# Optimization experiments

Hardware: AMD Instinct MI355X
Metric: run time of the kernel (lower is better)

Reference implementation:

```python
import jax, jax.numpy as jnp
import numpy as np
from jax import lax

B, N, C = 8, 100000, 90
H = W = 512
CONF_THR = 0.25
IOU_THR = 0.45
MAX_DET = 100  # fixed-size padded replacement for dynamic per-image NMS output


def setup_inputs() -> dict:
    key = jax.random.key(0)
    k1, k2, k3, k4, k5 = jax.random.split(key, 5)
    # small deltas so exp(dw), exp(dh) stay sane
    regression = jax.random.normal(k1, (B, N, 4), jnp.float32) * 0.1
    # shifted logits so sigmoid scores are mostly below conf_threshold (realistic sparsity)
    classification = jax.random.normal(k2, (B, N, C), jnp.float32) * 2.0 - 4.0
    # anchors in (y1, x1, y2, x2), valid boxes inside a 512x512 canvas
    cy = jax.random.uniform(k3, (1, N), minval=0.0, maxval=float(H))
    cx = jax.random.uniform(k4, (1, N), minval=0.0, maxval=float(W))
    hw = jax.random.uniform(k5, (1, N, 2), minval=16.0, maxval=128.0)
    hh, ww = hw[..., 0], hw[..., 1]
    anchors = jnp.stack([cy - hh / 2, cx - ww / 2, cy + hh / 2, cx + ww / 2], axis=-1)
    imgs = jnp.zeros((B, 3, H, W), jnp.float32)  # only shape (H, W) is used
    return {"regression": regression, "classification": classification,
            "anchors": anchors, "imgs": imgs}


def _bbox_transform(anchors, regression):
    y_c_a = (anchors[..., 0] + anchors[..., 2]) / 2
    x_c_a = (anchors[..., 1] + anchors[..., 3]) / 2
    ha = anchors[..., 2] - anchors[..., 0]
    wa = anchors[..., 3] - anchors[..., 1]
    w = jnp.exp(regression[..., 3]) * wa
    h = jnp.exp(regression[..., 2]) * ha
    y_c = regression[..., 0] * ha + y_c_a
    x_c = regression[..., 1] * wa + x_c_a
    # output in (x1, y1, x2, y2)
    return jnp.stack([x_c - w / 2, y_c - h / 2, x_c + w / 2, y_c + h / 2], axis=-1)


def _clip_boxes(boxes, height, width):
    x = jnp.clip(boxes[..., 0::2], 0.0, float(width))
    y = jnp.clip(boxes[..., 1::2], 0.0, float(height))
    return jnp.stack([x[..., 0], y[..., 0], x[..., 1], y[..., 1]], axis=-1)


def _iou_one_vs_all(box, boxes):
    # box [4], boxes [N,4] in x1y1x2y2
    x1 = jnp.maximum(box[0], boxes[:, 0])
    y1 = jnp.maximum(box[1], boxes[:, 1])
    x2 = jnp.minimum(box[2], boxes[:, 2])
    y2 = jnp.minimum(box[3], boxes[:, 3])
    inter = jnp.clip(x2 - x1, 0.0) * jnp.clip(y2 - y1, 0.0)
    area = (box[2] - box[0]) * (box[3] - box[1])
    areas = (boxes[:, 2] - boxes[:, 0]) * (boxes[:, 3] - boxes[:, 1])
    return inter / (area + areas - inter + 1e-8)


def _process_image(boxes, cls_logits):
    # boxes [N,4], cls_logits [N,C]
    scores_all = jax.nn.sigmoid(cls_logits)
    max_scores = jnp.max(scores_all, axis=1)
    labels = jnp.argmax(scores_all, axis=1)
    # below-threshold anchors get -1 so they can never be selected (== torch pre-NMS filter)
    s0 = jnp.where(max_scores > CONF_THR, max_scores, -1.0)
    s0 = lax.stop_gradient(s0)
    boxes_sg = lax.stop_gradient(boxes)

    def step(sc, _):
        best = jnp.argmax(sc)
        valid = sc[best] > 0.0
        iou = _iou_one_vs_all(boxes_sg[best], boxes_sg)
        sc = jnp.where(valid & (iou > IOU_THR), -1.0, sc)
        sc = sc.at[best].set(-1.0)
        return sc, jnp.where(valid, best, -1)

    _, idx = lax.scan(step, s0, None, length=MAX_DET)  # [MAX_DET] int
    valid = idx >= 0
    idx_safe = jnp.maximum(idx, 0)
    out_scores = jnp.where(valid, max_scores[idx_safe], 0.0)
    out_labels = jnp.where(valid, labels[idx_safe], -1)
    out_boxes = jnp.where(valid[:, None], boxes[idx_safe], 0.0)
    return out_scores, out_labels, out_boxes


def reference(regression, classification, anchors, imgs):
    height, width = imgs.shape[2], imgs.shape[3]
    boxes = _bbox_transform(anchors, regression)          # [B,N,4]
    boxes = _clip_boxes(boxes, height, width)
    scores, labels, det_boxes = jax.vmap(_process_image)(boxes, classification)
    # padded outputs: scores [B,MAX_DET], labels [B,MAX_DET] (-1 = invalid), boxes [B,MAX_DET,4]
    return scores, labels, det_boxes
```

## Files before the change

### kernel.cpp

```cpp
#include <hip/hip_runtime.h>

#define NB 8
#define NA 100000
#define NC 90
#define MAXDET 100
#define KCAND 2048
#define NBINS 4096
#define NBLK 13
#define BLK_ANCH 8000
#define ABLK 128
#define MASK_WORDS 32
#define CH_ROWS 64
#define CONF 0.25f
#define IOUT 0.45f

static constexpr size_t OFF_SCORE = 0;
static constexpr size_t OFF_LABEL = OFF_SCORE + (size_t)NB * NA * 4;
static constexpr size_t OFF_HROWS = OFF_LABEL + (size_t)NB * NA;
static constexpr size_t OFF_THR   = OFF_HROWS + (size_t)NB * NBLK * NBINS * 4;
static constexpr size_t OFF_CNT   = OFF_THR + 64;
static constexpr size_t OFF_CKEY  = OFF_CNT + 64;
static constexpr size_t OFF_SSC   = OFF_CKEY + (size_t)NB * KCAND * 8;
static constexpr size_t OFF_SLAB  = OFF_SSC + (size_t)NB * KCAND * 4;
static constexpr size_t OFF_SBOX  = OFF_SLAB + (size_t)NB * KCAND * 4;
static constexpr size_t OFF_MASK  = OFF_SBOX + (size_t)NB * KCAND * 16;

__device__ __forceinline__ float4 decode_clip(float4 a, float4 r) {
#pragma clang fp contract(off)
    float yca = (a.x + a.z) * 0.5f;
    float xca = (a.y + a.w) * 0.5f;
    float ha  = a.z - a.x;
    float wa  = a.w - a.y;
    float w   = expf(r.w) * wa;
    float h   = expf(r.z) * ha;
    float yc  = r.x * ha + yca;
    float xc  = r.y * wa + xca;
    float x1  = xc - w * 0.5f, y1 = yc - h * 0.5f;
    float x2  = xc + w * 0.5f, y2 = yc + h * 0.5f;
    x1 = fminf(fmaxf(x1, 0.0f), 512.0f);
    x2 = fminf(fmaxf(x2, 0.0f), 512.0f);
    y1 = fminf(fmaxf(y1, 0.0f), 512.0f);
    y2 = fminf(fmaxf(y2, 0.0f), 512.0f);
    return make_float4(x1, y1, x2, y2);
}

__global__ __launch_bounds__(256) void k_score_box(const float* __restrict__ cls,
                                                   float* __restrict__ ws_score,
                                                   unsigned char* __restrict__ ws_label) {
    __shared__ float tile[ABLK * NC];
    int t = threadIdx.x;
    const float4* g4 = (const float4*)(cls + (size_t)blockIdx.x * (ABLK * NC));
    float4* t4 = (float4*)tile;
    for (int i = t; i < ABLK * NC / 4; i += 256) t4[i] = g4[i];
    __syncthreads();

    int la = t >> 1, h = t & 1;
    const float* row = tile + la * NC + h * 45;
    int jbase = NC - 1 - h * 45;
    unsigned long long best = 0ULL;
    for (int j2 = 0; j2 < 45; ++j2) {
        float x = row[j2];
        float s = 1.0f / (1.0f + expf(-x));
        unsigned long long key = ((unsigned long long)__float_as_uint(s) << 32) |
                                 (unsigned long long)(unsigned)(jbase - j2);
        if (key > best) best = key;
    }
    unsigned long long o = __shfl_xor(best, 1, 64);
    if (o > best) best = o;
    if (h == 0) {
        int a = blockIdx.x * ABLK + la;
        ws_score[a] = __uint_as_float((unsigned)(best >> 32));
        ws_label[a] = (unsigned char)(NC - 1 - (unsigned)(best & 0xFFFFFFFFu));
    }
}

__global__ __launch_bounds__(256) void k_hist(const float* __restrict__ ws_score,
                                              unsigned* __restrict__ hrows) {
    __shared__ unsigned h[NBINS];
    int b = blockIdx.y, blk = blockIdx.x, tid = threadIdx.x;
    for (int i = tid; i < NBINS; i += 256) h[i] = 0u;
    __syncthreads();
    int base = blk * BLK_ANCH;
    int lim = min(BLK_ANCH, NA - base);
    const float* sc = ws_score + (size_t)b * NA + base;
    for (int i = tid; i < lim; i += 256) {
        float s = sc[i];
        if (s > CONF) {
            int bin = min((int)(s * (float)NBINS), NBINS - 1);
            atomicAdd(&h[bin], 1u);
        }
    }
    __syncthreads();
    unsigned* row = hrows + ((size_t)b * NBLK + blk) * NBINS;
    for (int i = tid; i < NBINS; i += 256) row[i] = h[i];
}

__global__ __launch_bounds__(256) void k_thresh(const unsigned* __restrict__ hrows,
                                                unsigned* __restrict__ thr_bin,
                                                unsigned* __restrict__ cnt) {
    __shared__ unsigned h[NBINS];
    __shared__ unsigned chunk[256];
    __shared__ int bstar;
    int b = blockIdx.x, t = threadIdx.x;
    for (int i = t; i < NBINS; i += 256) {
        unsigned s = 0;
        for (int r = 0; r < NBLK; ++r) s += hrows[((size_t)b * NBLK + r) * NBINS + i];
        h[i] = s;
    }
    if (t == 0) { bstar = NBINS - 1; cnt[b] = 0u; }
    __syncthreads();
    unsigned s = 0;
    for (int j = 0; j < 16; ++j) s += h[t * 16 + j];
    chunk[t] = s;
    __syncthreads();
    unsigned U = 0;
    for (int j = t + 1; j < 256; ++j) U += chunk[j];
    unsigned run = U;
    int cand = NBINS;
    for (int j = 15; j >= 0; --j) {
        run += h[t * 16 + j];
        if (run <= (unsigned)KCAND) cand = t * 16 + j;
    }
    if (cand < NBINS) atomicMin(&bstar, cand);
    __syncthreads();
    if (t == 0) thr_bin[b] = (unsigned)bstar;
}

__global__ __launch_bounds__(256) void k_compact(const float* __restrict__ ws_score,
                                                 const unsigned* __restrict__ thr_bin,
                                                 unsigned* __restrict__ cnt,
                                                 unsigned long long* __restrict__ ckey) {
    __shared__ unsigned scan[256];
    __shared__ unsigned base_s;
    int b = blockIdx.y, blk = blockIdx.x, t = threadIdx.x;
    int base = blk * BLK_ANCH;
    int lim = min(BLK_ANCH, NA - base);
    size_t ibase = (size_t)b * NA + base;
    unsigned thr = thr_bin[b];

    unsigned c = 0;
    for (int i = t; i < lim; i += 256) {
        float s = ws_score[ibase + i];
        if (s > CONF) {
            int bin = min((int)(s * (float)NBINS), NBINS - 1);
            if ((unsigned)bin >= thr) c++;
        }
    }
    scan[t] = c;
    __syncthreads();
    for (int off = 1; off < 256; off <<= 1) {
        unsigned v = (t >= off) ? scan[t - off] : 0u;
        __syncthreads();
        scan[t] += v;
        __syncthreads();
    }
    if (t == 255) base_s = atomicAdd(&cnt[b], scan[255]);
    __syncthreads();
    unsigned pos = base_s + scan[t] - c;
    for (int i = t; i < lim; i += 256) {
        float s = ws_score[ibase + i];
        if (s > CONF) {
            int bin = min((int)(s * (float)NBINS), NBINS - 1);
            if ((unsigned)bin >= thr) {
                unsigned p = pos++;
                if (p < (unsigned)KCAND) {
                    int n = base + i;
                    ckey[(size_t)b * KCAND + p] =
                        ((unsigned long long)__float_as_uint(s) << 32) |
                        (unsigned long long)(0xFFFFFFFFu - (unsigned)n);
                }
            }
        }
    }
}

__global__ __launch_bounds__(256) void k_sortdecode(const unsigned long long* __restrict__ ckey,
                                                    const unsigned* __restrict__ cnt,
                                                    const unsigned char* __restrict__ ws_label,
                                                    const float* __restrict__ reg,
                                                    const float* __restrict__ anc,
                                                    float* __restrict__ sscore,
                                                    int* __restrict__ slab,
                                                    float4* __restrict__ sbox) {
    __shared__ unsigned long long key[KCAND];
    int b = blockIdx.x, t = threadIdx.x;
    unsigned M = min(cnt[b], (unsigned)KCAND);
    for (int i = t; i < KCAND; i += 256)
        key[i] = (i < (int)M) ? ckey[(size_t)b * KCAND + i] : 0ULL;
    __syncthreads();
    for (int k = 2; k <= KCAND; k <<= 1) {
        for (int j = k >> 1; j > 0; j >>= 1) {
            for (int s = 0; s < KCAND / 256; ++s) {
                int p = t + s * 256;
                int q = p ^ j;
                if (q > p) {
                    unsigned long long a = key[p], bb = key[q];
                    bool desc = ((p & k) == 0);
                    if (desc ? (a < bb) : (a > bb)) { key[p] = bb; key[q] = a; }
                }
            }
            __syncthreads();
        }
    }
    for (int i = t; i < KCAND; i += 256) {
        unsigned long long kk = key[i];
        size_t o = (size_t)b * KCAND + i;
        if (kk != 0ULL) {
            unsigned n = 0xFFFFFFFFu - (unsigned)(kk & 0xFFFFFFFFu);
            sscore[o] = __uint_as_float((unsigned)(kk >> 32));
            slab[o] = (int)ws_label[(size_t)b * NA + n];
            float4 a4 = ((const float4*)anc)[n];
            float4 r4 = ((const float4*)reg)[(size_t)b * NA + n];
            sbox[o] = decode_clip(a4, r4);
        } else {
            sscore[o] = 0.0f;
            slab[o] = -1;
            sbox[o] = make_float4(0.f, 0.f, 0.f, 0.f);
        }
    }
}

__global__ __launch_bounds__(256) void k_mask(const float4* __restrict__ sbox,
                                              unsigned long long* __restrict__ mask) {
    __shared__ float4 bx[KCAND];
    int b = blockIdx.y, t = threadIdx.x;
    for (int i = t; i < KCAND; i += 256) bx[i] = sbox[(size_t)b * KCAND + i];
    __syncthreads();
    int r = t >> 5, w = t & 31;
    int row = blockIdx.x * 8 + r;
    float4 rb = bx[row];
    unsigned long long bits = 0ULL;
    {
#pragma clang fp contract(off)
        float areaR = (rb.z - rb.x) * (rb.w - rb.y);
        int cbase = w * 64;
        for (int cc = 0; cc < 64; ++cc) {
            float4 cb = bx[cbase + cc];
            float x1 = fmaxf(rb.x, cb.x), y1 = fmaxf(rb.y, cb.y);
            float x2 = fminf(rb.z, cb.z), y2 = fminf(rb.w, cb.w);
            float inter = fmaxf(x2 - x1, 0.0f) * fmaxf(y2 - y1, 0.0f);
            float areaC = (cb.z - cb.x) * (cb.w - cb.y);
            float iou = inter / (areaR + areaC - inter + 1e-8f);
            if (iou > IOUT) bits |= (1ULL << cc);
        }
    }
    mask[((size_t)b * KCAND + row) * MASK_WORDS + w] = bits;
}

__global__ __launch_bounds__(256) void k_scan(const unsigned long long* __restrict__ mask,
                                              const unsigned* __restrict__ cnt,
                                              const float* __restrict__ sscore,
                                              const int* __restrict__ slab,
                                              const float4* __restrict__ sbox,
                                              float* __restrict__ out) {
    __shared__ unsigned long long buf[2][CH_ROWS * MASK_WORDS];
    __shared__ int picks[MAXDET];
    __shared__ int npick_s;
    __shared__ int done_s;

    int b = blockIdx.x, t = threadIdx.x;
    unsigned M = min(cnt[b], (unsigned)KCAND);
    const unsigned long long* mbase = mask + (size_t)b * KCAND * MASK_WORDS;

    if (t == 0) { npick_s = 0; done_s = 0; }
    for (int i = t; i < CH_ROWS * MASK_WORDS; i += 256) buf[0][i] = mbase[i];
    __syncthreads();

    unsigned long long removed = 0ULL;
    int npick = 0;

    for (int q = 0; q < KCAND / CH_ROWS; ++q) {
        int cur = q & 1;
        bool havepre = (q + 1 < KCAND / CH_ROWS) && !done_s;
        unsigned long long pre[CH_ROWS * MASK_WORDS / 256];
        if (havepre) {
            const unsigned long long* src = mbase + (size_t)(q + 1) * CH_ROWS * MASK_WORDS;
#pragma unroll
            for (int s = 0; s < CH_ROWS * MASK_WORDS / 256; ++s) pre[s] = src[t + s * 256];
        }
        if (t < 64) {
            const unsigned long long* ch = buf[cur];
            int gstart = q * 64;
            if (gstart < (int)M && npick < MAXDET) {
                int vg = (int)M - gstart;
                unsigned long long valid = (vg >= 64) ? ~0ULL : ((1ULL << vg) - 1ULL);
                while (npick < MAXDET) {
                    unsigned long long rg = __shfl(removed, q, 64);
                    unsigned long long free = ~rg & valid;
                    if (free == 0ULL) break;
                    int cl = __ffsll((long long)free) - 1;
                    int c = gstart + cl;
                    if (t == 0) picks[npick] = c;
                    npick++;
                    if (t == q) removed |= (1ULL << cl);
                    if (t < 32) removed |= ch[cl * MASK_WORDS + t];
                }
            }
            if (t == 0) {
                npick_s = npick;
                done_s = (npick >= MAXDET || (q + 1) * CH_ROWS >= (int)M) ? 1 : 0;
            }
        }
        if (havepre) {
#pragma unroll
            for (int s = 0; s < CH_ROWS * MASK_WORDS / 256; ++s)
                buf[1 - cur][t + s * 256] = pre[s];
        }
        __syncthreads();
        if (done_s) break;
    }

    __syncthreads();
    int np = npick_s;
    for (int k = t; k < MAXDET; k += 256) {
        float sc = 0.0f, lb = -1.0f;
        float4 bb = make_float4(0.f, 0.f, 0.f, 0.f);
        if (k < np) {
            int i = picks[k];
            size_t o = (size_t)b * KCAND + i;
            sc = sscore[o];
            lb = (float)slab[o];
            bb = sbox[o];
        }
        out[b * MAXDET + k] = sc;
        out[NB * MAXDET + b * MAXDET + k] = lb;
        ((float4*)(out + 2 * NB * MAXDET))[b * MAXDET + k] = bb;
    }
}

extern "C" void kernel_launch(void* const* d_in, const int* in_sizes, int n_in,
                              void* d_out, int out_size, void* d_ws, size_t ws_size,
                              hipStream_t stream) {
    const float* reg = (const float*)d_in[0];
    const float* cls = (const float*)d_in[1];
    const float* anc = (const float*)d_in[2];

    char* ws = (char*)d_ws;
    float* ws_score           = (float*)(ws + OFF_SCORE);
    unsigned char* ws_label   = (unsigned char*)(ws + OFF_LABEL);
    unsigned* hrows           = (unsigned*)(ws + OFF_HROWS);
    unsigned* thr_bin         = (unsigned*)(ws + OFF_THR);
    unsigned* cnt             = (unsigned*)(ws + OFF_CNT);
    unsigned long long* ckey  = (unsigned long long*)(ws + OFF_CKEY);
    float* sscore             = (float*)(ws + OFF_SSC);
    int* slab                 = (int*)(ws + OFF_SLAB);
    float4* sbox              = (float4*)(ws + OFF_SBOX);
    unsigned long long* maskp = (unsigned long long*)(ws + OFF_MASK);

    float* out = (float*)d_out;

    k_score_box<<<NB * NA / ABLK, 256, 0, stream>>>(cls, ws_score, ws_label);
    k_hist<<<dim3(NBLK, NB), 256, 0, stream>>>(ws_score, hrows);
    k_thresh<<<NB, 256, 0, stream>>>(hrows, thr_bin, cnt);
    k_compact<<<dim3(NBLK, NB), 256, 0, stream>>>(ws_score, thr_bin, cnt, ckey);
    k_sortdecode<<<NB, 256, 0, stream>>>(ckey, cnt, ws_label, reg, anc, sscore, slab, sbox);
    k_mask<<<dim3(KCAND / 8, NB), 256, 0, stream>>>(sbox, maskp);
    k_scan<<<NB, 256, 0, stream>>>(maskp, cnt, sscore, slab, sbox, out);
}
```

Baseline: 608.0 us.

## Split score rows across four threads, widen sort block, simplify NMS scan

The score kernel now uses 64 anchors per block with four threads per anchor row and a two-step shuffle max, giving more blocks and shorter per-thread loops. The bitonic sort runs with 1024 threads per image instead of 256, so each thread does fewer compare-exchanges per stage. The NMS scan is replaced by a single-wave kernel that picks the next survivor with a ballot and reads mask rows straight from global memory, dropping the double-buffered shared-memory chunking. This removes barriers in the scan, but each pick now waits on a dependent global load.

New measurement: 580.7 us. 4.5% less time.

```diff
diff --git a/kernel.cpp b/kernel.cpp
--- a/kernel.cpp
+++ b/kernel.cpp
@@ -8,9 +8,8 @@
 #define NBINS 4096
 #define NBLK 13
 #define BLK_ANCH 8000
-#define ABLK 128
+#define ABLK 64
 #define MASK_WORDS 32
-#define CH_ROWS 64
 #define CONF 0.25f
 #define IOUT 0.45f
 
@@ -51,21 +50,25 @@
     int t = threadIdx.x;
     const float4* g4 = (const float4*)(cls + (size_t)blockIdx.x * (ABLK * NC));
     float4* t4 = (float4*)tile;
+#pragma unroll
     for (int i = t; i < ABLK * NC / 4; i += 256) t4[i] = g4[i];
     __syncthreads();
 
-    int la = t >> 1, h = t & 1;
-    const float* row = tile + la * NC + h * 45;
-    int jbase = NC - 1 - h * 45;
+    int la = t >> 2, h = t & 3;
+    int off = h * 22 + (h < 2 ? h : 2);
+    int len = (h < 2) ? 23 : 22;
+    const float* row = tile + la * NC + off;
     unsigned long long best = 0ULL;
-    for (int j2 = 0; j2 < 45; ++j2) {
-        float x = row[j2];
+    for (int i = 0; i < len; ++i) {
+        float x = row[i];
         float s = 1.0f / (1.0f + expf(-x));
         unsigned long long key = ((unsigned long long)__float_as_uint(s) << 32) |
-                                 (unsigned long long)(unsigned)(jbase - j2);
+                                 (unsigned long long)(unsigned)(NC - 1 - (off + i));
         if (key > best) best = key;
     }
     unsigned long long o = __shfl_xor(best, 1, 64);
+    if (o > best) best = o;
+    o = __shfl_xor(best, 2, 64);
     if (o > best) best = o;
     if (h == 0) {
         int a = blockIdx.x * ABLK + la;
@@ -174,24 +177,25 @@
     }
 }
 
-__global__ __launch_bounds__(256) void k_sortdecode(const unsigned long long* __restrict__ ckey,
-                                                    const unsigned* __restrict__ cnt,
-                                                    const unsigned char* __restrict__ ws_label,
-                                                    const float* __restrict__ reg,
-                                                    const float* __restrict__ anc,
-                                                    float* __restrict__ sscore,
-                                                    int* __restrict__ slab,
-                                                    float4* __restrict__ sbox) {
+__global__ __launch_bounds__(1024) void k_sortdecode(const unsigned long long* __restrict__ ckey,
+                                                     const unsigned* __restrict__ cnt,
+                                                     const unsigned char* __restrict__ ws_label,
+                                                     const float* __restrict__ reg,
+                                                     const float* __restrict__ anc,
+                                                     float* __restrict__ sscore,
+                                                     int* __restrict__ slab,
+                                                     float4* __restrict__ sbox) {
     __shared__ unsigned long long key[KCAND];
     int b = blockIdx.x, t = threadIdx.x;
     unsigned M = min(cnt[b], (unsigned)KCAND);
-    for (int i = t; i < KCAND; i += 256)
+    for (int i = t; i < KCAND; i += 1024)
         key[i] = (i < (int)M) ? ckey[(size_t)b * KCAND + i] : 0ULL;
     __syncthreads();
     for (int k = 2; k <= KCAND; k <<= 1) {
         for (int j = k >> 1; j > 0; j >>= 1) {
-            for (int s = 0; s < KCAND / 256; ++s) {
-                int p = t + s * 256;
+#pragma unroll
+            for (int s = 0; s < KCAND / 1024; ++s) {
+                int p = t + s * 1024;
                 int q = p ^ j;
                 if (q > p) {
                     unsigned long long a = key[p], bb = key[q];
@@ -202,7 +206,7 @@
             __syncthreads();
         }
     }
-    for (int i = t; i < KCAND; i += 256) {
+    for (int i = t; i < KCAND; i += 1024) {
         unsigned long long kk = key[i];
         size_t o = (size_t)b * KCAND + i;
         if (kk != 0ULL) {
@@ -247,72 +251,40 @@
     mask[((size_t)b * KCAND + row) * MASK_WORDS + w] = bits;
 }
 
-__global__ __launch_bounds__(256) void k_scan(const unsigned long long* __restrict__ mask,
-                                              const unsigned* __restrict__ cnt,
-                                              const float* __restrict__ sscore,
-                                              const int* __restrict__ slab,
-                                              const float4* __restrict__ sbox,
-                                              float* __restrict__ out) {
-    __shared__ unsigned long long buf[2][CH_ROWS * MASK_WORDS];
+__global__ __launch_bounds__(64) void k_scan(const unsigned long long* __restrict__ mask,
+                                             const unsigned* __restrict__ cnt,
+                                             const float* __restrict__ sscore,
+                                             const int* __restrict__ slab,
+                                             const float4* __restrict__ sbox,
+                                             float* __restrict__ out) {
     __shared__ int picks[MAXDET];
-    __shared__ int npick_s;
-    __shared__ int done_s;
-
-    int b = blockIdx.x, t = threadIdx.x;
+    int b = blockIdx.x, l = threadIdx.x;
     unsigned M = min(cnt[b], (unsigned)KCAND);
-    const unsigned long long* mbase = mask + (size_t)b * KCAND * MASK_WORDS;
-
-    if (t == 0) { npick_s = 0; done_s = 0; }
-    for (int i = t; i < CH_ROWS * MASK_WORDS; i += 256) buf[0][i] = mbase[i];
-    __syncthreads();
-
+    const unsigned long long* mb = mask + (size_t)b * KCAND * MASK_WORDS;
+
+    unsigned long long valid = 0ULL;
+    if (l < 32) {
+        int rem = (int)M - l * 64;
+        valid = (rem >= 64) ? ~0ULL : ((rem > 0) ? ((1ULL << rem) - 1ULL) : 0ULL);
+    }
     unsigned long long removed = 0ULL;
-    int npick = 0;
-
-    for (int q = 0; q < KCAND / CH_ROWS; ++q) {
-        int cur = q & 1;
-        bool havepre = (q + 1 < KCAND / CH_ROWS) && !done_s;
-        unsigned long long pre[CH_ROWS * MASK_WORDS / 256];
-        if (havepre) {
-            const unsigned long long* src = mbase + (size_t)(q + 1) * CH_ROWS * MASK_WORDS;
-#pragma unroll
-            for (int s = 0; s < CH_ROWS * MASK_WORDS / 256; ++s) pre[s] = src[t + s * 256];
-        }
-        if (t < 64) {
-            const unsigned long long* ch = buf[cur];
-            int gstart = q * 64;
-            if (gstart < (int)M && npick < MAXDET) {
-                int vg = (int)M - gstart;
-                unsigned long long valid = (vg >= 64) ? ~0ULL : ((1ULL << vg) - 1ULL);
-                while (npick < MAXDET) {
-                    unsigned long long rg = __shfl(removed, q, 64);
-                    unsigned long long free = ~rg & valid;
-                    if (free == 0ULL) break;
-                    int cl = __ffsll((long long)free) - 1;
-                    int c = gstart + cl;
-                    if (t == 0) picks[npick] = c;
-                    npick++;
-                    if (t == q) removed |= (1ULL << cl);
-                    if (t < 32) removed |= ch[cl * MASK_WORDS + t];
-                }
-            }
-            if (t == 0) {
-                npick_s = npick;
-                done_s = (npick >= MAXDET || (q + 1) * CH_ROWS >= (int)M) ? 1 : 0;
-            }
-        }
-        if (havepre) {
-#pragma unroll
-            for (int s = 0; s < CH_ROWS * MASK_WORDS / 256; ++s)
-                buf[1 - cur][t + s * 256] = pre[s];
-        }
-        __syncthreads();
-        if (done_s) break;
-    }
-
-    __syncthreads();
-    int np = npick_s;
-    for (int k = t; k < MAXDET; k += 256) {
+    int np = 0;
+    while (np < MAXDET) {
+        unsigned long long free = valid & ~removed;
+        unsigned long long act = __ballot(free != 0ULL);
+        if (act == 0ULL) break;
+        int lstar = __ffsll((long long)act) - 1;
+        unsigned long long fw = __shfl(free, lstar, 64);
+        int bit = __ffsll((long long)fw) - 1;
+        int c = lstar * 64 + bit;
+        if (l == 0) picks[np] = c;
+        np++;
+        if (l == lstar) removed |= (1ULL << bit);
+        if (l < 32) removed |= mb[(size_t)c * MASK_WORDS + l];
+    }
+    __syncthreads();
+
+    for (int k = l; k < MAXDET; k += 64) {
         float sc = 0.0f, lb = -1.0f;
         float4 bb = make_float4(0.f, 0.f, 0.f, 0.f);
         if (k < np) {
@@ -353,7 +325,7 @@
     k_hist<<<dim3(NBLK, NB), 256, 0, stream>>>(ws_score, hrows);
     k_thresh<<<NB, 256, 0, stream>>>(hrows, thr_bin, cnt);
     k_compact<<<dim3(NBLK, NB), 256, 0, stream>>>(ws_score, thr_bin, cnt, ckey);
-    k_sortdecode<<<NB, 256, 0, stream>>>(ckey, cnt, ws_label, reg, anc, sscore, slab, sbox);
+    k_sortdecode<<<NB, 1024, 0, stream>>>(ckey, cnt, ws_label, reg, anc, sscore, slab, sbox);
     k_mask<<<dim3(KCAND / 8, NB), 256, 0, stream>>>(sbox, maskp);
-    k_scan<<<NB, 256, 0, stream>>>(maskp, cnt, sscore, slab, sbox, out);
-}
+    k_scan<<<NB, 64, 0, stream>>>(maskp, cnt, sscore, slab, sbox, out);
+}
```
